# Optimization experiments

Measured on AMD Instinct MI355X. Metric: run time of the kernel, lower is better.

The kernel has to match this reference:

```python
import jax, jax.numpy as jnp
import numpy as np

H = 16
D = 64
EPS = 1e-6

def _phi(x):
    # elu_feature_map: elu(x) + 1
    return jax.nn.elu(x) + 1.0

def setup_inputs() -> dict:
    key = jax.random.key(0)
    k1, k2, k3, k4 = jax.random.split(key, 4)
    B, N = 4, 4096
    query = jax.random.normal(k1, (B, N, H * D), dtype=jnp.float32)
    key_t = jax.random.normal(k2, (B, N, H * D), dtype=jnp.float32)
    value = jax.random.normal(k3, (B, N, H * D), dtype=jnp.float32)
    W_out = jax.random.normal(k4, (D, H * D), dtype=jnp.float32) * (1.0 / np.sqrt(H * D))
    b_out = jnp.zeros((D,), dtype=jnp.float32)
    return {"query": query, "key": key_t, "value": value, "W_out": W_out, "b_out": b_out}

def reference(query, key, value, W_out, b_out):
    B, N, _ = query.shape
    # b n (h d) -> b h n d
    def split_heads(x):
        return x.reshape(B, N, H, D).transpose(0, 2, 1, 3)
    q = split_heads(query)
    k = split_heads(key)
    v = split_heads(value)
    Q = _phi(q)  # [B,H,N,D]
    K = _phi(k)
    # KV aggregation: O(N D^2)
    KV = jnp.einsum('bhnd,bhnm->bhdm', K, v)          # [B,H,D,D]
    Ksum = K.sum(axis=2)                               # [B,H,D]
    Z = 1.0 / (jnp.einsum('bhnd,bhd->bhn', Q, Ksum) + EPS)  # [B,H,N]
    out = jnp.einsum('bhnd,bhdm,bhn->bhnm', Q, KV, Z)  # [B,H,N,D]
    # b h n d -> b n h d -> (b*n, h*d)
    out = out.transpose(0, 2, 1, 3).reshape(B * N, H * D)
    return out @ W_out.T + b_out
```

## Files before the change

kernel.cpp:

```cpp
#include <hip/hip_runtime.h>

#define B_  4
#define N_  4096
#define H_  16
#define BH_ 64
#define S_  16
#define HS_ 4
#define ST_ 72
#define EPS_ 1e-6f

typedef _Float16 h2  __attribute__((ext_vector_type(2)));
typedef _Float16 h8  __attribute__((ext_vector_type(8)));
typedef float    f4v __attribute__((ext_vector_type(4)));

struct H2x2 { h2 a, b; };
struct H2x4 { h2 e[4]; };

__device__ __forceinline__ h8 ld_h8(const _Float16* p) {
    f4v r = *(const f4v*)p;
    return __builtin_bit_cast(h8, r);
}
__device__ __forceinline__ H2x4 ld_h2x4(const _Float16* p) {
    f4v r = *(const f4v*)p;
    return __builtin_bit_cast(H2x4, r);
}
__device__ __forceinline__ void st_h2x2(_Float16* p, h2 a, h2 b) {
    H2x2 t{a, b};
    *(float2*)p = __builtin_bit_cast(float2, t);
}
__device__ __forceinline__ float phi(float x) {
    return x > 0.0f ? x + 1.0f : __expf(x);
}
__device__ __forceinline__ float fdot2(h2 a, h2 b, float c) {
    return __builtin_amdgcn_fdot2(a, b, c, false);
}

__global__ __launch_bounds__(256) void k_kvpart(const float* __restrict__ K,
                                                const float* __restrict__ V,
                                                float* __restrict__ kvpart,
                                                float* __restrict__ kspart) {
    const int bh = blockIdx.x, s = blockIdx.y;
    const int b = bh >> 4, h = bh & 15;
    const int t = threadIdx.x, w = t >> 6, lane = t & 63;
    const int rp = t >> 4, c4 = t & 15;

    __shared__ __align__(16) _Float16 pool[2 * 2 * 64 * ST_];
    __shared__ float ksred[4][64];

    const f4v* Kf4 = (const f4v*)K;
    const f4v* Vf4 = (const f4v*)V;

    f4v kreg[4], vreg[4];
    auto LOAD = [&](int chunk) {
        const int n0 = s * (N_ / S_) + chunk * 64;
        size_t g = (size_t)(b * N_ + n0 + 4 * rp) * 256 + h * 16 + c4;
        kreg[0] = Kf4[g];       kreg[1] = Kf4[g + 256];
        kreg[2] = Kf4[g + 512]; kreg[3] = Kf4[g + 768];
        vreg[0] = Vf4[g];       vreg[1] = Vf4[g + 256];
        vreg[2] = Vf4[g + 512]; vreg[3] = Vf4[g + 768];
    };
    auto STORE = [&](int buf) {
        _Float16* Kt = pool + buf * (2 * 64 * ST_);
        _Float16* Vt = Kt + 64 * ST_;
#pragma unroll
        for (int dj = 0; dj < 4; ++dj) {
            int d = 4 * c4 + dj;
            h2 lo, hi;
            lo.x = (_Float16)phi(kreg[0][dj]); lo.y = (_Float16)phi(kreg[1][dj]);
            hi.x = (_Float16)phi(kreg[2][dj]); hi.y = (_Float16)phi(kreg[3][dj]);
            st_h2x2(&Kt[d * ST_ + 4 * rp], lo, hi);
            lo.x = (_Float16)vreg[0][dj]; lo.y = (_Float16)vreg[1][dj];
            hi.x = (_Float16)vreg[2][dj]; hi.y = (_Float16)vreg[3][dj];
            st_h2x2(&Vt[d * ST_ + 4 * rp], lo, hi);
        }
    };

    const int td0 = 2 * (w >> 1);
    const int tj0 = 2 * (w & 1);
    const int rA  = lane & 15;
    const int fo  = (lane >> 4) * 8;

    f4v acc[2][2];
#pragma unroll
    for (int a = 0; a < 2; ++a)
#pragma unroll
        for (int bb = 0; bb < 2; ++bb) acc[a][bb] = (f4v){0.f, 0.f, 0.f, 0.f};
    float ksum_acc = 0.f;
    h2 one2; one2.x = (_Float16)1.0f; one2.y = (_Float16)1.0f;

    LOAD(0);
    STORE(0);

    for (int chunk = 0; chunk < 4; ++chunk) {
        if (chunk + 1 < 4) LOAD(chunk + 1);
        __syncthreads();
        const int buf = chunk & 1;
        const _Float16* Kt = pool + buf * (2 * 64 * ST_);
        const _Float16* Vt = Kt + 64 * ST_;
#pragma unroll
        for (int ks = 0; ks < 2; ++ks) {
            h8 a0 = ld_h8(&Kt[(16 * (td0 + 0) + rA) * ST_ + ks * 32 + fo]);
            h8 a1 = ld_h8(&Kt[(16 * (td0 + 1) + rA) * ST_ + ks * 32 + fo]);
            h8 b0 = ld_h8(&Vt[(16 * (tj0 + 0) + rA) * ST_ + ks * 32 + fo]);
            h8 b1 = ld_h8(&Vt[(16 * (tj0 + 1) + rA) * ST_ + ks * 32 + fo]);
            acc[0][0] = __builtin_amdgcn_mfma_f32_16x16x32_f16(a0, b0, acc[0][0], 0, 0, 0);
            acc[0][1] = __builtin_amdgcn_mfma_f32_16x16x32_f16(a0, b1, acc[0][1], 0, 0, 0);
            acc[1][0] = __builtin_amdgcn_mfma_f32_16x16x32_f16(a1, b0, acc[1][0], 0, 0, 0);
            acc[1][1] = __builtin_amdgcn_mfma_f32_16x16x32_f16(a1, b1, acc[1][1], 0, 0, 0);
        }
        {
            int d = t & 63, qtr = t >> 6;
            H2x4 x0 = ld_h2x4(&Kt[d * ST_ + qtr * 16]);
            H2x4 x1 = ld_h2x4(&Kt[d * ST_ + qtr * 16 + 8]);
#pragma unroll
            for (int i = 0; i < 4; ++i) {
                ksum_acc = fdot2(x0.e[i], one2, ksum_acc);
                ksum_acc = fdot2(x1.e[i], one2, ksum_acc);
            }
        }
        if (chunk + 1 < 4) STORE((chunk + 1) & 1);
    }

    float* outp = kvpart + (size_t)(bh * S_ + s) * 4096;
#pragma unroll
    for (int a = 0; a < 2; ++a)
#pragma unroll
        for (int bb = 0; bb < 2; ++bb)
#pragma unroll
            for (int r = 0; r < 4; ++r) {
                int d = 16 * (td0 + a) + (lane >> 4) * 4 + r;
                int m = 16 * (tj0 + bb) + (lane & 15);
                outp[d * 64 + m] = acc[a][bb][r];
            }
    ksred[t >> 6][t & 63] = ksum_acc;
    __syncthreads();
    if (t < 64) {
        kspart[(size_t)(bh * S_ + s) * 64 + t] =
            ksred[0][t] + ksred[1][t] + ksred[2][t] + ksred[3][t];
    }
}

__global__ __launch_bounds__(256) void k_makeM(const float* __restrict__ kvpart,
                                               const float* __restrict__ kspart,
                                               const float* __restrict__ W,
                                               _Float16* __restrict__ Mt,
                                               float* __restrict__ Ksum) {
    const int bh = blockIdx.x;
    const int h  = bh & 15;
    const int t  = threadIdx.x;

    __shared__ float KVs[64][68];
    __shared__ float Ws[64][68];

    const f4v* kv4 = (const f4v*)kvpart;
    const f4v* W4  = (const f4v*)W;

    for (int idx = t; idx < 1024; idx += 256) {
        int row = idx >> 4, c4 = idx & 15;
        f4v r = {0.f, 0.f, 0.f, 0.f};
#pragma unroll 4
        for (int s = 0; s < S_; ++s) {
            f4v a = kv4[(size_t)(bh * S_ + s) * 1024 + idx];
            r += a;
        }
        *(f4v*)&KVs[row][c4 * 4] = r;
        *(f4v*)&Ws[row][c4 * 4] = W4[(size_t)row * 256 + h * 16 + c4];
    }
    if (t < 64) {
        float ks = 0.f;
        for (int s = 0; s < S_; ++s) ks += kspart[(size_t)(bh * S_ + s) * 64 + t];
        Ksum[(size_t)bh * 64 + t] = ks;
    }
    __syncthreads();

    const int jbase = (t >> 4) * 4, dbase = (t & 15) * 4;
    float acc[4][4] = {{0.f}};
#pragma unroll 4
    for (int m4 = 0; m4 < 16; ++m4) {
        f4v wr[4], kvr[4];
#pragma unroll
        for (int j = 0; j < 4; ++j) wr[j] = *(const f4v*)&Ws[jbase + j][m4 * 4];
#pragma unroll
        for (int i = 0; i < 4; ++i) kvr[i] = *(const f4v*)&KVs[dbase + i][m4 * 4];
#pragma unroll
        for (int j = 0; j < 4; ++j)
#pragma unroll
            for (int i = 0; i < 4; ++i)
                acc[j][i] += wr[j][0] * kvr[i][0] + wr[j][1] * kvr[i][1] +
                             wr[j][2] * kvr[i][2] + wr[j][3] * kvr[i][3];
    }
#pragma unroll
    for (int j = 0; j < 4; ++j) {
        h2 lo, hi;
        lo.x = (_Float16)acc[j][0]; lo.y = (_Float16)acc[j][1];
        hi.x = (_Float16)acc[j][2]; hi.y = (_Float16)acc[j][3];
        H2x2 pk{lo, hi};
        *(float2*)&Mt[((size_t)bh * 64 + jbase + j) * 64 + dbase] =
            __builtin_bit_cast(float2, pk);
    }
}

__global__ __launch_bounds__(256) void k_out(const float* __restrict__ Q,
                                             const _Float16* __restrict__ Mtg,
                                             const float* __restrict__ Ksum,
                                             float* __restrict__ outpart) {
    const int nc = blockIdx.x, b = blockIdx.y, hs = blockIdx.z;
    const int n0 = nc * 64;
    const int t = threadIdx.x, w = t >> 6, lane = t & 63;
    const int rp4 = t >> 4, c4 = t & 15;

    __shared__ __align__(16) _Float16 pool[2 * 2 * 64 * ST_];
    __shared__ float zz[64];
    __shared__ h2 Kss[2][32];

    const f4v* Qf4 = (const f4v*)Q;

    f4v qr[4], mr[2];
    float ksa = 0.f, ksb = 0.f;
    auto LOAD = [&](int hh) {
        const int h = hs * 4 + hh, bh = b * 16 + h;
        size_t g = (size_t)(b * N_ + n0 + rp4) * 256 + h * 16 + c4;
        qr[0] = Qf4[g];            qr[1] = Qf4[g + 16 * 256];
        qr[2] = Qf4[g + 32 * 256]; qr[3] = Qf4[g + 48 * 256];
        mr[0] = ((const f4v*)Mtg)[(size_t)bh * 512 + t];
        mr[1] = ((const f4v*)Mtg)[(size_t)bh * 512 + t + 256];
        if (t < 32) {
            ksa = Ksum[(size_t)bh * 64 + 2 * t];
            ksb = Ksum[(size_t)bh * 64 + 2 * t + 1];
        }
    };
    auto STORE = [&](int buf) {
        _Float16* Qp = pool + buf * (2 * 64 * ST_);
        _Float16* Mt = Qp + 64 * ST_;
#pragma unroll
        for (int r = 0; r < 4; ++r) {
            int row = rp4 + 16 * r;
            h2 p0, p1;
            p0.x = (_Float16)phi(qr[r][0]); p0.y = (_Float16)phi(qr[r][1]);
            p1.x = (_Float16)phi(qr[r][2]); p1.y = (_Float16)phi(qr[r][3]);
            st_h2x2(&Qp[row * ST_ + 4 * c4], p0, p1);
        }
        *(f4v*)&Mt[(t >> 3) * ST_ + (t & 7) * 8] = mr[0];
        *(f4v*)&Mt[((t + 256) >> 3) * ST_ + (t & 7) * 8] = mr[1];
        if (t < 32) { h2 kk; kk.x = (_Float16)ksa; kk.y = (_Float16)ksb; Kss[buf][t] = kk; }
    };

    const int tn0 = 2 * (w >> 1), tj0 = 2 * (w & 1);
    const int rA = lane & 15, fo = (lane >> 4) * 8;
    float facc[2][2][4] = {{{0.f}}};

    LOAD(0);
    STORE(0);

    for (int hh = 0; hh < 4; ++hh) {
        if (hh + 1 < 4) LOAD(hh + 1);
        __syncthreads();
        const int buf = hh & 1;
        const _Float16* Qp = pool + buf * (2 * 64 * ST_);
        const _Float16* Mt = Qp + 64 * ST_;

        if (t < 64) {
            float zp = 0.f;
#pragma unroll
            for (int c = 0; c < 8; ++c) {
                H2x4 x = ld_h2x4(&Qp[t * ST_ + c * 8]);
#pragma unroll
                for (int i = 0; i < 4; ++i) zp = fdot2(x.e[i], Kss[buf][c * 4 + i], zp);
            }
            zz[t] = 1.0f / (zp + EPS_);
        }
        __syncthreads();

        f4v acc[2][2];
#pragma unroll
        for (int a = 0; a < 2; ++a)
#pragma unroll
            for (int bb = 0; bb < 2; ++bb) acc[a][bb] = (f4v){0.f, 0.f, 0.f, 0.f};
#pragma unroll
        for (int ks = 0; ks < 2; ++ks) {
            h8 a0 = ld_h8(&Qp[(16 * (tn0 + 0) + rA) * ST_ + ks * 32 + fo]);
            h8 a1 = ld_h8(&Qp[(16 * (tn0 + 1) + rA) * ST_ + ks * 32 + fo]);
            h8 b0 = ld_h8(&Mt[(16 * (tj0 + 0) + rA) * ST_ + ks * 32 + fo]);
            h8 b1 = ld_h8(&Mt[(16 * (tj0 + 1) + rA) * ST_ + ks * 32 + fo]);
            acc[0][0] = __builtin_amdgcn_mfma_f32_16x16x32_f16(a0, b0, acc[0][0], 0, 0, 0);
            acc[0][1] = __builtin_amdgcn_mfma_f32_16x16x32_f16(a0, b1, acc[0][1], 0, 0, 0);
            acc[1][0] = __builtin_amdgcn_mfma_f32_16x16x32_f16(a1, b0, acc[1][0], 0, 0, 0);
            acc[1][1] = __builtin_amdgcn_mfma_f32_16x16x32_f16(a1, b1, acc[1][1], 0, 0, 0);
        }
#pragma unroll
        for (int a = 0; a < 2; ++a)
#pragma unroll
            for (int r = 0; r < 4; ++r) {
                int row = 16 * (tn0 + a) + (lane >> 4) * 4 + r;
                float z = zz[row];
                facc[a][0][r] += z * acc[a][0][r];
                facc[a][1][r] += z * acc[a][1][r];
            }
        if (hh + 1 < 4) STORE((hh + 1) & 1);
    }

    float* op = outpart + (size_t)hs * (B_ * N_ * 64);
#pragma unroll
    for (int a = 0; a < 2; ++a)
#pragma unroll
        for (int bb = 0; bb < 2; ++bb)
#pragma unroll
            for (int r = 0; r < 4; ++r) {
                int n = 16 * (tn0 + a) + (lane >> 4) * 4 + r;
                int j = 16 * (tj0 + bb) + (lane & 15);
                op[(size_t)(b * N_ + n0 + n) * 64 + j] = facc[a][bb][r];
            }
}

__global__ __launch_bounds__(256) void k_red(const float* __restrict__ outpart,
                                             const float* __restrict__ bout,
                                             float* __restrict__ out) {
    const int p = blockIdx.x * 256 + threadIdx.x;
    const f4v* P4 = (const f4v*)outpart;
    const f4v* B4 = (const f4v*)bout;
    f4v o = B4[p & 15];
    const int stride = B_ * N_ * 64 / 4;
#pragma unroll
    for (int hs = 0; hs < HS_; ++hs) o += P4[(size_t)hs * stride + p];
    ((f4v*)out)[p] = o;
}

extern "C" void kernel_launch(void* const* d_in, const int* in_sizes, int n_in,
                              void* d_out, int out_size, void* d_ws, size_t ws_size,
                              hipStream_t stream) {
    const float* q  = (const float*)d_in[0];
    const float* k  = (const float*)d_in[1];
    const float* v  = (const float*)d_in[2];
    const float* W  = (const float*)d_in[3];
    const float* bo = (const float*)d_in[4];
    float* out = (float*)d_out;

    float* ws      = (float*)d_ws;
    float* kvpart  = ws;
    float* kspart  = kvpart + (size_t)BH_ * S_ * 4096;
    float* Mt      = kspart + (size_t)BH_ * S_ * 64;
    float* Ksum    = Mt + (size_t)BH_ * 4096 / 2;
    float* outpart = Ksum + (size_t)BH_ * 64;

    k_kvpart<<<dim3(BH_, S_), 256, 0, stream>>>(k, v, kvpart, kspart);
    k_makeM<<<BH_, 256, 0, stream>>>(kvpart, kspart, W, (_Float16*)Mt, Ksum);
    k_out<<<dim3(N_ / 64, B_, HS_), 256, 0, stream>>>(q, (const _Float16*)Mt, Ksum, outpart);
    k_red<<<B_ * N_ * 64 / 4 / 256, 256, 0, stream>>>(outpart, bo, out);
}
```

Baseline: 230.0 us.

## Deepen kvpart prefetch, split makeM across d-quarters, use lightweight LDS barriers

k_kvpart now holds two register sets and issues global loads two chunks ahead in a fully unrolled schedule, so memory latency overlaps more compute. k_makeM is launched with four times as many blocks, each producing a 16-column slice of M, which raises parallelism for that small kernel. The cost is that W is reloaded by every block. Several __syncthreads are replaced with an explicit lgkmcnt wait plus s_barrier that skips the vmcnt drain, at the risk of subtle ordering bugs if a global load result is consumed across that barrier.

```diff
diff --git a/kernel.cpp b/kernel.cpp
--- a/kernel.cpp
+++ b/kernel.cpp
@@ -34,6 +34,11 @@
 __device__ __forceinline__ float fdot2(h2 a, h2 b, float c) {
     return __builtin_amdgcn_fdot2(a, b, c, false);
 }
+__device__ __forceinline__ void barrier_lgkm() {
+    asm volatile("s_waitcnt lgkmcnt(0)" ::: "memory");
+    __builtin_amdgcn_sched_barrier(0);
+    __builtin_amdgcn_s_barrier();
+}
 
 __global__ __launch_bounds__(256) void k_kvpart(const float* __restrict__ K,
                                                 const float* __restrict__ V,
@@ -50,8 +55,9 @@
     const f4v* Kf4 = (const f4v*)K;
     const f4v* Vf4 = (const f4v*)V;
 
-    f4v kreg[4], vreg[4];
-    auto LOAD = [&](int chunk) {
+    f4v kA[4], vA[4], kB[4], vB[4];
+
+    auto LOADX = [&](f4v* kreg, f4v* vreg, int chunk) {
         const int n0 = s * (N_ / S_) + chunk * 64;
         size_t g = (size_t)(b * N_ + n0 + 4 * rp) * 256 + h * 16 + c4;
         kreg[0] = Kf4[g];       kreg[1] = Kf4[g + 256];
@@ -59,7 +65,7 @@
         vreg[0] = Vf4[g];       vreg[1] = Vf4[g + 256];
         vreg[2] = Vf4[g + 512]; vreg[3] = Vf4[g + 768];
     };
-    auto STORE = [&](int buf) {
+    auto STOREX = [&](const f4v* kreg, const f4v* vreg, int buf) {
         _Float16* Kt = pool + buf * (2 * 64 * ST_);
         _Float16* Vt = Kt + 64 * ST_;
 #pragma unroll
@@ -88,13 +94,7 @@
     float ksum_acc = 0.f;
     h2 one2; one2.x = (_Float16)1.0f; one2.y = (_Float16)1.0f;
 
-    LOAD(0);
-    STORE(0);
-
-    for (int chunk = 0; chunk < 4; ++chunk) {
-        if (chunk + 1 < 4) LOAD(chunk + 1);
-        __syncthreads();
-        const int buf = chunk & 1;
+    auto COMPUTE = [&](int buf) {
         const _Float16* Kt = pool + buf * (2 * 64 * ST_);
         const _Float16* Vt = Kt + 64 * ST_;
 #pragma unroll
@@ -118,8 +118,24 @@
                 ksum_acc = fdot2(x1.e[i], one2, ksum_acc);
             }
         }
-        if (chunk + 1 < 4) STORE((chunk + 1) & 1);
-    }
+    };
+
+    LOADX(kA, vA, 0);
+    LOADX(kB, vB, 1);
+    STOREX(kA, vA, 0);
+    barrier_lgkm();
+    LOADX(kA, vA, 2);
+    COMPUTE(0);
+    STOREX(kB, vB, 1);
+    barrier_lgkm();
+    LOADX(kB, vB, 3);
+    COMPUTE(1);
+    STOREX(kA, vA, 0);
+    barrier_lgkm();
+    COMPUTE(0);
+    STOREX(kB, vB, 1);
+    barrier_lgkm();
+    COMPUTE(1);
 
     float* outp = kvpart + (size_t)(bh * S_ + s) * 4096;
 #pragma unroll
@@ -145,59 +161,55 @@
                                                const float* __restrict__ W,
                                                _Float16* __restrict__ Mt,
                                                float* __restrict__ Ksum) {
-    const int bh = blockIdx.x;
+    const int bh = blockIdx.x, dq = blockIdx.y;
     const int h  = bh & 15;
     const int t  = threadIdx.x;
 
-    __shared__ float KVs[64][68];
+    __shared__ float KVs[16][68];
     __shared__ float Ws[64][68];
 
     const f4v* kv4 = (const f4v*)kvpart;
     const f4v* W4  = (const f4v*)W;
 
-    for (int idx = t; idx < 1024; idx += 256) {
-        int row = idx >> 4, c4 = idx & 15;
+    {
+        int row = t >> 4, c4 = t & 15;
         f4v r = {0.f, 0.f, 0.f, 0.f};
 #pragma unroll 4
-        for (int s = 0; s < S_; ++s) {
-            f4v a = kv4[(size_t)(bh * S_ + s) * 1024 + idx];
-            r += a;
-        }
+        for (int s = 0; s < S_; ++s)
+            r += kv4[(size_t)(bh * S_ + s) * 1024 + (dq * 16 + row) * 16 + c4];
         *(f4v*)&KVs[row][c4 * 4] = r;
-        *(f4v*)&Ws[row][c4 * 4] = W4[(size_t)row * 256 + h * 16 + c4];
-    }
-    if (t < 64) {
+    }
+    for (int idx = t; idx < 1024; idx += 256) {
+        int wrow = idx >> 4, wc = idx & 15;
+        *(f4v*)&Ws[wrow][wc * 4] = W4[(size_t)wrow * 256 + h * 16 + wc];
+    }
+    if (dq == 0 && t < 64) {
         float ks = 0.f;
         for (int s = 0; s < S_; ++s) ks += kspart[(size_t)(bh * S_ + s) * 64 + t];
         Ksum[(size_t)bh * 64 + t] = ks;
     }
     __syncthreads();
 
-    const int jbase = (t >> 4) * 4, dbase = (t & 15) * 4;
-    float acc[4][4] = {{0.f}};
+    const int j = t >> 2, dl = (t & 3) * 4;
+    float acc[4] = {0.f, 0.f, 0.f, 0.f};
 #pragma unroll 4
     for (int m4 = 0; m4 < 16; ++m4) {
-        f4v wr[4], kvr[4];
-#pragma unroll
-        for (int j = 0; j < 4; ++j) wr[j] = *(const f4v*)&Ws[jbase + j][m4 * 4];
-#pragma unroll
-        for (int i = 0; i < 4; ++i) kvr[i] = *(const f4v*)&KVs[dbase + i][m4 * 4];
-#pragma unroll
-        for (int j = 0; j < 4; ++j)
-#pragma unroll
-            for (int i = 0; i < 4; ++i)
-                acc[j][i] += wr[j][0] * kvr[i][0] + wr[j][1] * kvr[i][1] +
-                             wr[j][2] * kvr[i][2] + wr[j][3] * kvr[i][3];
-    }
-#pragma unroll
-    for (int j = 0; j < 4; ++j) {
-        h2 lo, hi;
-        lo.x = (_Float16)acc[j][0]; lo.y = (_Float16)acc[j][1];
-        hi.x = (_Float16)acc[j][2]; hi.y = (_Float16)acc[j][3];
-        H2x2 pk{lo, hi};
-        *(float2*)&Mt[((size_t)bh * 64 + jbase + j) * 64 + dbase] =
-            __builtin_bit_cast(float2, pk);
-    }
+        f4v wr  = *(const f4v*)&Ws[j][m4 * 4];
+        f4v kv0 = *(const f4v*)&KVs[dl + 0][m4 * 4];
+        f4v kv1 = *(const f4v*)&KVs[dl + 1][m4 * 4];
+        f4v kv2 = *(const f4v*)&KVs[dl + 2][m4 * 4];
+        f4v kv3 = *(const f4v*)&KVs[dl + 3][m4 * 4];
+        acc[0] += wr[0] * kv0[0] + wr[1] * kv0[1] + wr[2] * kv0[2] + wr[3] * kv0[3];
+        acc[1] += wr[0] * kv1[0] + wr[1] * kv1[1] + wr[2] * kv1[2] + wr[3] * kv1[3];
+        acc[2] += wr[0] * kv2[0] + wr[1] * kv2[1] + wr[2] * kv2[2] + wr[3] * kv2[3];
+        acc[3] += wr[0] * kv3[0] + wr[1] * kv3[1] + wr[2] * kv3[2] + wr[3] * kv3[3];
+    }
+    h2 lo, hi;
+    lo.x = (_Float16)acc[0]; lo.y = (_Float16)acc[1];
+    hi.x = (_Float16)acc[2]; hi.y = (_Float16)acc[3];
+    H2x2 pk{lo, hi};
+    *(float2*)&Mt[((size_t)bh * 64 + j) * 64 + dq * 16 + dl] =
+        __builtin_bit_cast(float2, pk);
 }
 
 __global__ __launch_bounds__(256) void k_out(const float* __restrict__ Q,
@@ -254,7 +266,7 @@
 
     for (int hh = 0; hh < 4; ++hh) {
         if (hh + 1 < 4) LOAD(hh + 1);
-        __syncthreads();
+        barrier_lgkm();
         const int buf = hh & 1;
         const _Float16* Qp = pool + buf * (2 * 64 * ST_);
         const _Float16* Mt = Qp + 64 * ST_;
@@ -269,7 +281,7 @@
             }
             zz[t] = 1.0f / (zp + EPS_);
         }
-        __syncthreads();
+        barrier_lgkm();
 
         f4v acc[2][2];
 #pragma unroll
@@ -343,7 +355,7 @@
     float* outpart = Ksum + (size_t)BH_ * 64;
 
     k_kvpart<<<dim3(BH_, S_), 256, 0, stream>>>(k, v, kvpart, kspart);
-    k_makeM<<<BH_, 256, 0, stream>>>(kvpart, kspart, W, (_Float16*)Mt, Ksum);
+    k_makeM<<<dim3(BH_, 4), 256, 0, stream>>>(kvpart, kspart, W, (_Float16*)Mt, Ksum);
     k_out<<<dim3(N_ / 64, B_, HS_), 256, 0, stream>>>(q, (const _Float16*)Mt, Ksum, outpart);
     k_red<<<B_ * N_ * 64 / 4 / 256, 256, 0, stream>>>(outpart, bo, out);
 }
```

Result: no change. 226.0 us (-1.8%).
